# Kernel tuning notes

Hardware: AMD Instinct MI355X
Metric: run time of the kernel (lower is better)

Reference implementation:

```python
import jax, jax.numpy as jnp
import numpy as np
import math

B, L, C = 8, 1024, 256
H, CH = 8, 32  # num_heads, c_hidden; H*CH == C


def setup_inputs() -> dict:
    key = jax.random.key(0)
    ks = jax.random.split(key, 8)
    s = 0.02
    return {
        "q_x": jax.random.normal(ks[0], (B, L, C), jnp.float32),
        "bias_mask": jnp.zeros((B, 1, 1, L), jnp.float32),
        "bias_pair": jax.random.normal(ks[1], (B, H, L, L), jnp.float32),
        "Wq": jax.random.normal(ks[2], (C, H * CH), jnp.float32) * s,
        "Wk": jax.random.normal(ks[3], (C, H * CH), jnp.float32) * s,
        "Wv": jax.random.normal(ks[4], (C, H * CH), jnp.float32) * s,
        "Wg": jax.random.normal(ks[5], (C, H * CH), jnp.float32) * s,
        "bg": jnp.ones((H * CH,), jnp.float32),  # gating bias init = 1 in AlphaFold
        "Wo": jax.random.normal(ks[6], (H * CH, C), jnp.float32) * s,
        "bo": jnp.zeros((C,), jnp.float32),
    }


def reference(q_x, bias_mask, bias_pair, Wq, Wk, Wv, Wg, bg, Wo, bo):
    # QKV projections (self-attention: kv_x = q_x), split heads -> [B, H, L, CH]
    def proj(W):
        return (q_x @ W).reshape(B, L, H, CH).transpose(0, 2, 1, 3)

    q = proj(Wq) / math.sqrt(CH)
    k = proj(Wk)
    v = proj(Wv)

    # scores + multi-bias add, stable softmax over keys
    a = jnp.einsum("bhqc,bhkc->bhqk", q, k) + bias_mask + bias_pair
    a = jax.nn.softmax(a, axis=-1)

    # weighted values -> [B, L, H, CH]
    o = jnp.einsum("bhqk,bhkc->bhqc", a, v).transpose(0, 2, 1, 3)

    # sigmoid gating from query data
    g = jax.nn.sigmoid(q_x @ Wg + bg).reshape(B, L, H, CH)
    o = o * g

    # merge heads and output projection
    o = o.reshape(B, L, H * CH)
    return o @ Wo + bo
```

## Files before the change

kernel.cpp:

```cpp
#include <hip/hip_runtime.h>
#include <hip/hip_bf16.h>
#include <hip/hip_fp16.h>
#include <math.h>

#define BB 8
#define LL 1024
#define CC 256
#define HH 8
#define CHD 32

typedef __attribute__((ext_vector_type(8))) _Float16 half8;
typedef __attribute__((ext_vector_type(4))) float f32x4;
typedef __attribute__((ext_vector_type(4))) unsigned int u32x4;

#define MFMA16 __builtin_amdgcn_mfma_f32_16x16x32_f16
#define LO_SCALE 2048.f
#define LO_INV   4.8828125e-4f

__device__ __forceinline__ float u2f(unsigned short u) {
    return __uint_as_float(((unsigned)u) << 16);
}
__device__ __forceinline__ float ldv(const void* p, size_t i, bool f32) {
    return f32 ? ((const float*)p)[i] : u2f(((const unsigned short*)p)[i]);
}
__device__ __forceinline__ float4 ldv4(const void* p, size_t i, bool f32) {
    if (f32) return *(const float4*)((const float*)p + i);
    ushort4 u = *(const ushort4*)((const unsigned short*)p + i);
    return make_float4(u2f(u.x), u2f(u.y), u2f(u.z), u2f(u.w));
}
__device__ __forceinline__ bool probe_f32(const void* bg) {
    return *(const unsigned*)bg == 0x3F800000u;
}
__device__ __forceinline__ unsigned pack_h2(float a, float b) {
    __half2 h = __floats2half2_rn(a, b);
    return *(unsigned*)&h;
}
__device__ __forceinline__ void store_h4(__half* p, float a, float b, float c, float d) {
    uint2 u = make_uint2(pack_h2(a, b), pack_h2(c, d));
    *(uint2*)p = u;
}
__device__ __forceinline__ void cvt_store_hilo(__half* ph, __half* pl, float4 v) {
    __half2 a = __floats2half2_rn(v.x, v.y), b2 = __floats2half2_rn(v.z, v.w);
    *(uint2*)ph = make_uint2(*(unsigned*)&a, *(unsigned*)&b2);
    float rx = (v.x - __low2float(a))  * LO_SCALE;
    float ry = (v.y - __high2float(a)) * LO_SCALE;
    float rz = (v.z - __low2float(b2)) * LO_SCALE;
    float rw = (v.w - __high2float(b2)) * LO_SCALE;
    __half2 c = __floats2half2_rn(rx, ry), d = __floats2half2_rn(rz, rw);
    *(uint2*)pl = make_uint2(*(unsigned*)&c, *(unsigned*)&d);
}

__global__ __launch_bounds__(256) void prep_w_kernel(
    const void* __restrict__ Wq, const void* __restrict__ Wk,
    const void* __restrict__ Wv, const void* __restrict__ Wg,
    const void* __restrict__ Wo, const void* __restrict__ bg,
    __half* __restrict__ wt_hi, __half* __restrict__ wt_lo)
{
    const bool f32 = probe_f32(bg);
    const int blk = blockIdx.x;
    const int mi = blk >> 6, tile = blk & 63;
    const void* W = (mi == 0) ? Wq : (mi == 1) ? Wk : (mi == 2) ? Wv
                  : (mi == 3) ? Wg : Wo;
    const int tr = tile >> 3, tc = tile & 7;
    __shared__ float ts[32][33];
    const int t = threadIdx.x;
    for (int e = t; e < 1024; e += 256) {
        const int r = e >> 5, c = e & 31;
        ts[r][c] = ldv(W, (size_t)(32 * tr + r) * 256 + 32 * tc + c, f32);
    }
    __syncthreads();
    for (int e = t; e < 1024; e += 256) {
        const int r = e >> 5, c = e & 31;
        const float v = ts[c][r];
        const __half h = __float2half(v);
        const __half l = __float2half((v - __half2float(h)) * LO_SCALE);
        const size_t o = (size_t)mi * 65536 + (size_t)(32 * tc + r) * 256 + 32 * tr + c;
        wt_hi[o] = h;
        wt_lo[o] = l;
    }
}

__global__ __launch_bounds__(256) void proj_mfma_kernel(
    const void* __restrict__ qx,
    const __half* __restrict__ wt_hi, const __half* __restrict__ wt_lo,
    const void* __restrict__ bg,
    __half* __restrict__ q_ws, __half* __restrict__ k_ws,
    __half* __restrict__ vt_ws, __half* __restrict__ g_ws)
{
    const bool f32 = probe_f32(bg);
    __shared__ __align__(16) __half xhi[16][264];
    __shared__ __align__(16) __half xlo[16][264];
    const int t  = threadIdx.x;
    const int m0 = blockIdx.x * 16;

    for (int e = t; e < 1024; e += 256) {
        const int r = e >> 6, c4 = e & 63;
        float4 v = ldv4(qx, (size_t)(m0 + r) * CC + (size_t)c4 * 4, f32);
        cvt_store_hilo(&xhi[r][c4 * 4], &xlo[r][c4 * 4], v);
    }
    __syncthreads();

    const int ln = t & 63, mat = t >> 6;
    const int lq = ln & 15, g = ln >> 4;
    const __half* bh_base = wt_hi + (size_t)mat * 65536 + (size_t)lq * 256 + 8 * g;
    const __half* bl_base = wt_lo + (size_t)mat * 65536 + (size_t)lq * 256 + 8 * g;

    f32x4 accm[16], accc[16];
#pragma unroll
    for (int nt = 0; nt < 16; ++nt) {
        accm[nt] = (f32x4){0.f, 0.f, 0.f, 0.f};
        accc[nt] = (f32x4){0.f, 0.f, 0.f, 0.f};
    }

    const bool vmat = (mat == 2);
    for (int kc = 0; kc < 8; ++kc) {
        const half8 ah = *(const half8*)&xhi[lq][kc * 32 + 8 * g];
        const half8 al = *(const half8*)&xlo[lq][kc * 32 + 8 * g];
#pragma unroll
        for (int nt = 0; nt < 16; ++nt) {
            const half8 bh = *(const half8*)(bh_base + nt * 4096 + kc * 32);
            const half8 bl = *(const half8*)(bl_base + nt * 4096 + kc * 32);
            if (!vmat) {
                accm[nt] = MFMA16(bh, ah, accm[nt], 0, 0, 0);
                accc[nt] = MFMA16(bl, ah, accc[nt], 0, 0, 0);
                accc[nt] = MFMA16(bh, al, accc[nt], 0, 0, 0);
            } else {
                accm[nt] = MFMA16(ah, bh, accm[nt], 0, 0, 0);
                accc[nt] = MFMA16(al, bh, accc[nt], 0, 0, 0);
                accc[nt] = MFMA16(ah, bl, accc[nt], 0, 0, 0);
            }
        }
    }

    const int b  = m0 >> 10;
    const int l0 = m0 & 1023;

    if (mat == 3) {
        const int m = m0 + lq;
#pragma unroll
        for (int nt = 0; nt < 16; ++nt) {
            const int n0 = nt * 16 + 4 * g;
            float4 bgv = ldv4(bg, n0, f32);
            float z0 = accm[nt].x + accc[nt].x * LO_INV + bgv.x;
            float z1 = accm[nt].y + accc[nt].y * LO_INV + bgv.y;
            float z2 = accm[nt].z + accc[nt].z * LO_INV + bgv.z;
            float z3 = accm[nt].w + accc[nt].w * LO_INV + bgv.w;
            store_h4(g_ws + (size_t)m * 256 + n0,
                     1.f / (1.f + __expf(-z0)), 1.f / (1.f + __expf(-z1)),
                     1.f / (1.f + __expf(-z2)), 1.f / (1.f + __expf(-z3)));
        }
    } else if (vmat) {
#pragma unroll
        for (int nt = 0; nt < 16; ++nt) {
            const int n = nt * 16 + lq, h = n >> 5, ch = n & 31;
            __half* dst = vt_ws + ((size_t)(b * HH + h) * CHD + ch) * LL + l0 + 4 * g;
            store_h4(dst,
                     accm[nt].x + accc[nt].x * LO_INV,
                     accm[nt].y + accc[nt].y * LO_INV,
                     accm[nt].z + accc[nt].z * LO_INV,
                     accm[nt].w + accc[nt].w * LO_INV);
        }
    } else {
        const float scale = (mat == 0) ? 0.17677669529663687f : 1.f;
        __half* dst0 = (mat == 0) ? q_ws : k_ws;
        const int l = l0 + lq;
#pragma unroll
        for (int nt = 0; nt < 16; ++nt) {
            const int n0 = nt * 16 + 4 * g, h = n0 >> 5, ch = n0 & 31;
            __half* dst = dst0 + ((size_t)(b * HH + h) * LL + l) * CHD + ch;
            store_h4(dst,
                     (accm[nt].x + accc[nt].x * LO_INV) * scale,
                     (accm[nt].y + accc[nt].y * LO_INV) * scale,
                     (accm[nt].z + accc[nt].z * LO_INV) * scale,
                     (accm[nt].w + accc[nt].w * LO_INV) * scale);
        }
    }
}

__global__ __launch_bounds__(256) void attn_mfma_kernel(
    const __half* __restrict__ q_ws, const __half* __restrict__ k_ws,
    const __half* __restrict__ vt_ws, const __half* __restrict__ g_ws,
    const void* __restrict__ mask, const void* __restrict__ bias,
    const void* __restrict__ bg,
    float* __restrict__ og_out)
{
    const bool f32 = probe_f32(bg);
    const int t  = threadIdx.x;
    const int wv = t >> 6;
    const int ln = t & 63;
    const int lq = ln & 15;
    const int g  = ln >> 4;
    const int bh = blockIdx.y;
    const int b  = bh >> 3, h = bh & 7;
    const int q0 = blockIdx.x * 64 + wv * 16;
    const int qi = q0 + lq;

    const half8 qfrag = *(const half8*)(q_ws + ((size_t)bh * LL + qi) * CHD + 8 * g);

    f32x4 o0 = {0.f, 0.f, 0.f, 0.f};
    f32x4 o1 = {0.f, 0.f, 0.f, 0.f};
    float m_run = -1e30f, l_run = 0.f;

    const size_t bias_base = ((size_t)bh * LL + qi) * LL;
    const size_t mask_base = (size_t)b * LL;
    const f32x4 zz = {0.f, 0.f, 0.f, 0.f};

    for (int k0 = 0; k0 < LL; k0 += 64) {
        f32x4 sc[4];
#pragma unroll
        for (int s = 0; s < 4; ++s) {
            half8 kf = *(const half8*)(k_ws +
                ((size_t)bh * LL + k0 + 16 * s + lq) * CHD + 8 * g);
            sc[s] = MFMA16(kf, qfrag, zz, 0, 0, 0);
        }
#pragma unroll
        for (int s = 0; s < 4; ++s) {
            const int kk = k0 + 16 * s + 4 * g;
            float4 b4 = ldv4(bias, bias_base + kk, f32);
            float4 m4 = ldv4(mask, mask_base + kk, f32);
            sc[s].x += b4.x + m4.x;
            sc[s].y += b4.y + m4.y;
            sc[s].z += b4.z + m4.z;
            sc[s].w += b4.w + m4.w;
        }
        float mt = fmaxf(fmaxf(sc[0].x, sc[0].y), fmaxf(sc[0].z, sc[0].w));
#pragma unroll
        for (int s = 1; s < 4; ++s)
            mt = fmaxf(mt, fmaxf(fmaxf(sc[s].x, sc[s].y), fmaxf(sc[s].z, sc[s].w)));
        mt = fmaxf(mt, __shfl_xor(mt, 16));
        mt = fmaxf(mt, __shfl_xor(mt, 32));
        const float mn = fmaxf(m_run, mt);
        const float alpha = __expf(m_run - mn);
        m_run = mn;
        float ls = 0.f;
#pragma unroll
        for (int s = 0; s < 4; ++s) {
            sc[s].x = __expf(sc[s].x - mn); ls += sc[s].x;
            sc[s].y = __expf(sc[s].y - mn); ls += sc[s].y;
            sc[s].z = __expf(sc[s].z - mn); ls += sc[s].z;
            sc[s].w = __expf(sc[s].w - mn); ls += sc[s].w;
        }
        ls += __shfl_xor(ls, 16);
        ls += __shfl_xor(ls, 32);
        l_run = l_run * alpha + ls;
        o0 = o0 * alpha;
        o1 = o1 * alpha;

        unsigned ph[4][2];
#pragma unroll
        for (int s = 0; s < 4; ++s) {
            ph[s][0] = pack_h2(sc[s].x, sc[s].y);
            ph[s][1] = pack_h2(sc[s].z, sc[s].w);
        }
#pragma unroll
        for (int tt = 0; tt < 2; ++tt) {
            unsigned bfr[4];
#pragma unroll
            for (int w = 0; w < 4; ++w) {
                const int src = lq + 16 * (2 * (g & 1) + (w >> 1));
                unsigned lo = (unsigned)__shfl((int)ph[2 * tt + 0][w & 1], src);
                unsigned hi = (unsigned)__shfl((int)ph[2 * tt + 1][w & 1], src);
                bfr[w] = (g >= 2) ? hi : lo;
            }
            u32x4 bv = {bfr[0], bfr[1], bfr[2], bfr[3]};
            half8 pB = __builtin_bit_cast(half8, bv);
            half8 vf0 = *(const half8*)(vt_ws +
                ((size_t)bh * CHD + lq) * LL + k0 + 32 * tt + 8 * g);
            o0 = MFMA16(vf0, pB, o0, 0, 0, 0);
            half8 vf1 = *(const half8*)(vt_ws +
                ((size_t)bh * CHD + 16 + lq) * LL + k0 + 32 * tt + 8 * g);
            o1 = MFMA16(vf1, pB, o1, 0, 0, 0);
        }
    }

    const float inv = 1.f / l_run;
    const size_t row = (size_t)b * LL + qi;
    const __half* gp = g_ws + row * CC + h * CHD + 4 * g;
    float* op = og_out + row * CC + h * CHD + 4 * g;
    float4 r0, r1;
    r0.x = o0.x * inv * __half2float(gp[0]);
    r0.y = o0.y * inv * __half2float(gp[1]);
    r0.z = o0.z * inv * __half2float(gp[2]);
    r0.w = o0.w * inv * __half2float(gp[3]);
    r1.x = o1.x * inv * __half2float(gp[16]);
    r1.y = o1.y * inv * __half2float(gp[17]);
    r1.z = o1.z * inv * __half2float(gp[18]);
    r1.w = o1.w * inv * __half2float(gp[19]);
    *(float4*)op = r0;
    *(float4*)(op + 16) = r1;
}

__global__ __launch_bounds__(256) void out_mfma_kernel(
    float* __restrict__ io,
    const __half* __restrict__ wt_hi, const __half* __restrict__ wt_lo,
    const void* __restrict__ bo, const void* __restrict__ bg)
{
    const bool f32 = probe_f32(bg);
    __shared__ __align__(16) __half xhi[16][264];
    __shared__ __align__(16) __half xlo[16][264];
    const int t  = threadIdx.x;
    const int m0 = blockIdx.x * 16;

    for (int e = t; e < 1024; e += 256) {
        const int r = e >> 6, c4 = e & 63;
        float4 v = *(const float4*)(io + (size_t)(m0 + r) * CC + (size_t)c4 * 4);
        cvt_store_hilo(&xhi[r][c4 * 4], &xlo[r][c4 * 4], v);
    }
    __syncthreads();

    const int ln = t & 63, wv = t >> 6;
    const int lq = ln & 15, g = ln >> 4;
    const __half* bh_base = wt_hi + (size_t)4 * 65536 + (size_t)lq * 256 + 8 * g;
    const __half* bl_base = wt_lo + (size_t)4 * 65536 + (size_t)lq * 256 + 8 * g;

    f32x4 accm[4], accc[4];
#pragma unroll
    for (int j = 0; j < 4; ++j) {
        accm[j] = (f32x4){0.f, 0.f, 0.f, 0.f};
        accc[j] = (f32x4){0.f, 0.f, 0.f, 0.f};
    }

    for (int kc = 0; kc < 8; ++kc) {
        const half8 ah = *(const half8*)&xhi[lq][kc * 32 + 8 * g];
        const half8 al = *(const half8*)&xlo[lq][kc * 32 + 8 * g];
#pragma unroll
        for (int j = 0; j < 4; ++j) {
            const int nt = wv * 4 + j;
            const half8 bh = *(const half8*)(bh_base + nt * 4096 + kc * 32);
            const half8 bl = *(const half8*)(bl_base + nt * 4096 + kc * 32);
            accm[j] = MFMA16(bh, ah, accm[j], 0, 0, 0);
            accc[j] = MFMA16(bl, ah, accc[j], 0, 0, 0);
            accc[j] = MFMA16(bh, al, accc[j], 0, 0, 0);
        }
    }

    const int m = m0 + lq;
#pragma unroll
    for (int j = 0; j < 4; ++j) {
        const int n0 = (wv * 4 + j) * 16 + 4 * g;
        float4 bov = ldv4(bo, n0, f32);
        float4 r;
        r.x = accm[j].x + accc[j].x * LO_INV + bov.x;
        r.y = accm[j].y + accc[j].y * LO_INV + bov.y;
        r.z = accm[j].z + accc[j].z * LO_INV + bov.z;
        r.w = accm[j].w + accc[j].w * LO_INV + bov.w;
        *(float4*)(io + (size_t)m * 256 + n0) = r;
    }
}

extern "C" void kernel_launch(void* const* d_in, const int* in_sizes, int n_in,
                              void* d_out, int out_size, void* d_ws, size_t ws_size,
                              hipStream_t stream) {
    const void* qx   = d_in[0];
    const void* mask = d_in[1];
    const void* bias = d_in[2];
    const void* Wq   = d_in[3];
    const void* Wk   = d_in[4];
    const void* Wv   = d_in[5];
    const void* Wg   = d_in[6];
    const void* bg   = d_in[7];
    const void* Wo   = d_in[8];
    const void* bo   = d_in[9];
    float* out = (float*)d_out;

    char* ws = (char*)d_ws;
    const size_t TEN = (size_t)BB * LL * CC * sizeof(__half);
    __half* q_ws  = (__half*)(ws + 0 * TEN);
    __half* k_ws  = (__half*)(ws + 1 * TEN);
    __half* vt_ws = (__half*)(ws + 2 * TEN);
    __half* g_ws  = (__half*)(ws + 3 * TEN);
    __half* wt_hi = (__half*)(ws + 4 * TEN);
    __half* wt_lo = (__half*)(ws + 4 * TEN + (size_t)2 * 1024 * 1024);

    prep_w_kernel<<<dim3(320), 256, 0, stream>>>(Wq, Wk, Wv, Wg, Wo, bg,
                                                 wt_hi, wt_lo);
    proj_mfma_kernel<<<dim3(512), 256, 0, stream>>>(qx, wt_hi, wt_lo, bg,
                                                    q_ws, k_ws, vt_ws, g_ws);
    attn_mfma_kernel<<<dim3(16, 64), 256, 0, stream>>>(q_ws, k_ws, vt_ws, g_ws,
                                                       mask, bias, bg, out);
    out_mfma_kernel<<<dim3(512), 256, 0, stream>>>(out, wt_hi, wt_lo, bo, bg);
}
```

Baseline: 519.6 us.

## Retile projection GEMM per matrix and prefetch pair bias in attention

The projection kernel now launches one block per (32-row tile, matrix). Each wave covers 64 output columns across two 16-row subtiles, so every loaded weight fragment is reused twice and the per-wave accumulator count drops from 32 to 16 vectors. The input tile is converted to hi/lo halves four times per row (once per matrix) instead of once, which adds some redundant staging. Separately, the attention loop software-prefetches the next 64-column chunk of the pair bias into registers to hide the latency of the dominant HBM stream, at the cost of extra live registers.

New measurement: 484.0 us. -6.8%, faster.

```diff
diff --git a/kernel.cpp b/kernel.cpp
--- a/kernel.cpp
+++ b/kernel.cpp
@@ -88,46 +88,60 @@
     __half* __restrict__ vt_ws, __half* __restrict__ g_ws)
 {
     const bool f32 = probe_f32(bg);
-    __shared__ __align__(16) __half xhi[16][264];
-    __shared__ __align__(16) __half xlo[16][264];
-    const int t  = threadIdx.x;
-    const int m0 = blockIdx.x * 16;
-
-    for (int e = t; e < 1024; e += 256) {
+    __shared__ __align__(16) __half xhi[32][264];
+    __shared__ __align__(16) __half xlo[32][264];
+    const int t   = threadIdx.x;
+    const int m0  = blockIdx.x * 32;
+    const int mat = blockIdx.y;
+
+    for (int e = t; e < 2048; e += 256) {
         const int r = e >> 6, c4 = e & 63;
         float4 v = ldv4(qx, (size_t)(m0 + r) * CC + (size_t)c4 * 4, f32);
         cvt_store_hilo(&xhi[r][c4 * 4], &xlo[r][c4 * 4], v);
     }
     __syncthreads();
 
-    const int ln = t & 63, mat = t >> 6;
+    const int ln = t & 63, wv = t >> 6;
     const int lq = ln & 15, g = ln >> 4;
-    const __half* bh_base = wt_hi + (size_t)mat * 65536 + (size_t)lq * 256 + 8 * g;
-    const __half* bl_base = wt_lo + (size_t)mat * 65536 + (size_t)lq * 256 + 8 * g;
-
-    f32x4 accm[16], accc[16];
-#pragma unroll
-    for (int nt = 0; nt < 16; ++nt) {
-        accm[nt] = (f32x4){0.f, 0.f, 0.f, 0.f};
-        accc[nt] = (f32x4){0.f, 0.f, 0.f, 0.f};
-    }
+    const int nb = 64 * wv;
+    const __half* bh_base = wt_hi + (size_t)mat * 65536
+                          + (size_t)(nb + lq) * 256 + 8 * g;
+    const __half* bl_base = wt_lo + (size_t)mat * 65536
+                          + (size_t)(nb + lq) * 256 + 8 * g;
+
+    f32x4 accm[2][4], accc[2][4];
+#pragma unroll
+    for (int ms = 0; ms < 2; ++ms)
+#pragma unroll
+        for (int j = 0; j < 4; ++j) {
+            accm[ms][j] = (f32x4){0.f, 0.f, 0.f, 0.f};
+            accc[ms][j] = (f32x4){0.f, 0.f, 0.f, 0.f};
+        }
 
     const bool vmat = (mat == 2);
+#pragma unroll
     for (int kc = 0; kc < 8; ++kc) {
-        const half8 ah = *(const half8*)&xhi[lq][kc * 32 + 8 * g];
-        const half8 al = *(const half8*)&xlo[lq][kc * 32 + 8 * g];
-#pragma unroll
-        for (int nt = 0; nt < 16; ++nt) {
-            const half8 bh = *(const half8*)(bh_base + nt * 4096 + kc * 32);
-            const half8 bl = *(const half8*)(bl_base + nt * 4096 + kc * 32);
-            if (!vmat) {
-                accm[nt] = MFMA16(bh, ah, accm[nt], 0, 0, 0);
-                accc[nt] = MFMA16(bl, ah, accc[nt], 0, 0, 0);
-                accc[nt] = MFMA16(bh, al, accc[nt], 0, 0, 0);
-            } else {
-                accm[nt] = MFMA16(ah, bh, accm[nt], 0, 0, 0);
-                accc[nt] = MFMA16(al, bh, accc[nt], 0, 0, 0);
-                accc[nt] = MFMA16(ah, bl, accc[nt], 0, 0, 0);
+        half8 bh[4], bl[4];
+#pragma unroll
+        for (int j = 0; j < 4; ++j) {
+            bh[j] = *(const half8*)(bh_base + j * 4096 + kc * 32);
+            bl[j] = *(const half8*)(bl_base + j * 4096 + kc * 32);
+        }
+#pragma unroll
+        for (int ms = 0; ms < 2; ++ms) {
+            const half8 ah = *(const half8*)&xhi[ms * 16 + lq][kc * 32 + 8 * g];
+            const half8 al = *(const half8*)&xlo[ms * 16 + lq][kc * 32 + 8 * g];
+#pragma unroll
+            for (int j = 0; j < 4; ++j) {
+                if (!vmat) {
+                    accm[ms][j] = MFMA16(bh[j], ah, accm[ms][j], 0, 0, 0);
+                    accc[ms][j] = MFMA16(bl[j], ah, accc[ms][j], 0, 0, 0);
+                    accc[ms][j] = MFMA16(bh[j], al, accc[ms][j], 0, 0, 0);
+                } else {
+                    accm[ms][j] = MFMA16(ah, bh[j], accm[ms][j], 0, 0, 0);
+                    accc[ms][j] = MFMA16(al, bh[j], accc[ms][j], 0, 0, 0);
+                    accc[ms][j] = MFMA16(ah, bl[j], accc[ms][j], 0, 0, 0);
+                }
             }
         }
     }
@@ -136,43 +150,52 @@
     const int l0 = m0 & 1023;
 
     if (mat == 3) {
-        const int m = m0 + lq;
-#pragma unroll
-        for (int nt = 0; nt < 16; ++nt) {
-            const int n0 = nt * 16 + 4 * g;
-            float4 bgv = ldv4(bg, n0, f32);
-            float z0 = accm[nt].x + accc[nt].x * LO_INV + bgv.x;
-            float z1 = accm[nt].y + accc[nt].y * LO_INV + bgv.y;
-            float z2 = accm[nt].z + accc[nt].z * LO_INV + bgv.z;
-            float z3 = accm[nt].w + accc[nt].w * LO_INV + bgv.w;
-            store_h4(g_ws + (size_t)m * 256 + n0,
-                     1.f / (1.f + __expf(-z0)), 1.f / (1.f + __expf(-z1)),
-                     1.f / (1.f + __expf(-z2)), 1.f / (1.f + __expf(-z3)));
+#pragma unroll
+        for (int ms = 0; ms < 2; ++ms) {
+            const int m = m0 + ms * 16 + lq;
+#pragma unroll
+            for (int j = 0; j < 4; ++j) {
+                const int n0 = nb + 16 * j + 4 * g;
+                float4 bgv = ldv4(bg, n0, f32);
+                float z0 = accm[ms][j].x + accc[ms][j].x * LO_INV + bgv.x;
+                float z1 = accm[ms][j].y + accc[ms][j].y * LO_INV + bgv.y;
+                float z2 = accm[ms][j].z + accc[ms][j].z * LO_INV + bgv.z;
+                float z3 = accm[ms][j].w + accc[ms][j].w * LO_INV + bgv.w;
+                store_h4(g_ws + (size_t)m * 256 + n0,
+                         1.f / (1.f + __expf(-z0)), 1.f / (1.f + __expf(-z1)),
+                         1.f / (1.f + __expf(-z2)), 1.f / (1.f + __expf(-z3)));
+            }
         }
     } else if (vmat) {
 #pragma unroll
-        for (int nt = 0; nt < 16; ++nt) {
-            const int n = nt * 16 + lq, h = n >> 5, ch = n & 31;
-            __half* dst = vt_ws + ((size_t)(b * HH + h) * CHD + ch) * LL + l0 + 4 * g;
-            store_h4(dst,
-                     accm[nt].x + accc[nt].x * LO_INV,
-                     accm[nt].y + accc[nt].y * LO_INV,
-                     accm[nt].z + accc[nt].z * LO_INV,
-                     accm[nt].w + accc[nt].w * LO_INV);
-        }
+        for (int ms = 0; ms < 2; ++ms)
+#pragma unroll
+            for (int j = 0; j < 4; ++j) {
+                const int n = nb + 16 * j + lq, h = n >> 5, ch = n & 31;
+                __half* dst = vt_ws + ((size_t)(b * HH + h) * CHD + ch) * LL
+                            + l0 + ms * 16 + 4 * g;
+                store_h4(dst,
+                         accm[ms][j].x + accc[ms][j].x * LO_INV,
+                         accm[ms][j].y + accc[ms][j].y * LO_INV,
+                         accm[ms][j].z + accc[ms][j].z * LO_INV,
+                         accm[ms][j].w + accc[ms][j].w * LO_INV);
+            }
     } else {
         const float scale = (mat == 0) ? 0.17677669529663687f : 1.f;
         __half* dst0 = (mat == 0) ? q_ws : k_ws;
-        const int l = l0 + lq;
-#pragma unroll
-        for (int nt = 0; nt < 16; ++nt) {
-            const int n0 = nt * 16 + 4 * g, h = n0 >> 5, ch = n0 & 31;
-            __half* dst = dst0 + ((size_t)(b * HH + h) * LL + l) * CHD + ch;
-            store_h4(dst,
-                     (accm[nt].x + accc[nt].x * LO_INV) * scale,
-                     (accm[nt].y + accc[nt].y * LO_INV) * scale,
-                     (accm[nt].z + accc[nt].z * LO_INV) * scale,
-                     (accm[nt].w + accc[nt].w * LO_INV) * scale);
+#pragma unroll
+        for (int ms = 0; ms < 2; ++ms) {
+            const int l = l0 + ms * 16 + lq;
+#pragma unroll
+            for (int j = 0; j < 4; ++j) {
+                const int n0 = nb + 16 * j + 4 * g, h = n0 >> 5, ch = n0 & 31;
+                __half* dst = dst0 + ((size_t)(b * HH + h) * LL + l) * CHD + ch;
+                store_h4(dst,
+                         (accm[ms][j].x + accc[ms][j].x * LO_INV) * scale,
+                         (accm[ms][j].y + accc[ms][j].y * LO_INV) * scale,
+                         (accm[ms][j].z + accc[ms][j].z * LO_INV) * scale,
+                         (accm[ms][j].w + accc[ms][j].w * LO_INV) * scale);
+            }
         }
     }
 }
@@ -205,6 +228,11 @@
     const size_t mask_base = (size_t)b * LL;
     const f32x4 zz = {0.f, 0.f, 0.f, 0.f};
 
+    float4 b4c[4];
+#pragma unroll
+    for (int s = 0; s < 4; ++s)
+        b4c[s] = ldv4(bias, bias_base + 16 * s + 4 * g, f32);
+
     for (int k0 = 0; k0 < LL; k0 += 64) {
         f32x4 sc[4];
 #pragma unroll
@@ -213,15 +241,18 @@
                 ((size_t)bh * LL + k0 + 16 * s + lq) * CHD + 8 * g);
             sc[s] = MFMA16(kf, qfrag, zz, 0, 0, 0);
         }
+        const int kn = (k0 + 64 < LL) ? (k0 + 64) : k0;
+        float4 b4n[4];
+#pragma unroll
+        for (int s = 0; s < 4; ++s)
+            b4n[s] = ldv4(bias, bias_base + kn + 16 * s + 4 * g, f32);
 #pragma unroll
         for (int s = 0; s < 4; ++s) {
-            const int kk = k0 + 16 * s + 4 * g;
-            float4 b4 = ldv4(bias, bias_base + kk, f32);
-            float4 m4 = ldv4(mask, mask_base + kk, f32);
-            sc[s].x += b4.x + m4.x;
-            sc[s].y += b4.y + m4.y;
-            sc[s].z += b4.z + m4.z;
-            sc[s].w += b4.w + m4.w;
+            float4 m4 = ldv4(mask, mask_base + k0 + 16 * s + 4 * g, f32);
+            sc[s].x += b4c[s].x + m4.x;
+            sc[s].y += b4c[s].y + m4.y;
+            sc[s].z += b4c[s].z + m4.z;
+            sc[s].w += b4c[s].w + m4.w;
         }
         float mt = fmaxf(fmaxf(sc[0].x, sc[0].y), fmaxf(sc[0].z, sc[0].w));
 #pragma unroll
@@ -271,6 +302,8 @@
                 ((size_t)bh * CHD + 16 + lq) * LL + k0 + 32 * tt + 8 * g);
             o1 = MFMA16(vf1, pB, o1, 0, 0, 0);
         }
+#pragma unroll
+        for (int s = 0; s < 4; ++s) b4c[s] = b4n[s];
     }
 
     const float inv = 1.f / l_run;
@@ -374,8 +407,8 @@
 
     prep_w_kernel<<<dim3(320), 256, 0, stream>>>(Wq, Wk, Wv, Wg, Wo, bg,
                                                  wt_hi, wt_lo);
-    proj_mfma_kernel<<<dim3(512), 256, 0, stream>>>(qx, wt_hi, wt_lo, bg,
-                                                    q_ws, k_ws, vt_ws, g_ws);
+    proj_mfma_kernel<<<dim3(256, 4), 256, 0, stream>>>(qx, wt_hi, wt_lo, bg,
+                                                       q_ws, k_ws, vt_ws, g_ws);
     attn_mfma_kernel<<<dim3(16, 64), 256, 0, stream>>>(q_ws, k_ws, vt_ws, g_ws,
                                                        mask, bias, bg, out);
     out_mfma_kernel<<<dim3(512), 256, 0, stream>>>(out, wt_hi, wt_lo, bo, bg);
```
